# Performance work log

Measured on AMD Instinct MI355X. Metric: run time of the kernel, lower is better.

The kernel has to match this reference:

```python
import jax, jax.numpy as jnp
import numpy as np

B, T, S, D, H, HD, DFF, NB = 2, 2048, 2048, 768, 12, 64, 3072, 32
HID = H * HD
EPS = 1e-6
NEG = -1e9


def rmsnorm(x, w):
    # T5 RMSNorm: no mean subtraction, no bias
    var = jnp.mean(jnp.square(x), axis=-1, keepdims=True)
    return x * jax.lax.rsqrt(var + EPS) * w


def sdpa(h, kv, m, wq, wk, wv, wo):
    # h: [B,Tq,D], kv: [B,Tk,D], m: additive mask broadcastable to [B,H,Tq,Tk]
    b, tq, _ = h.shape
    tk = kv.shape[1]
    q = (h @ wq).reshape(b, tq, H, HD)
    k = (kv @ wk).reshape(b, tk, H, HD)
    v = (kv @ wv).reshape(b, tk, H, HD)
    scores = jnp.einsum('bthd,bshd->bhts', q, k) + m  # scale=1.0 (T5)
    p = jax.nn.softmax(scores, axis=-1)
    y = jnp.einsum('bhts,bshd->bthd', p, v).reshape(b, tq, HID)
    return y @ wo


def setup_inputs() -> dict:
    key = jax.random.key(0)
    ks = jax.random.split(key, 16)
    x = jax.random.normal(ks[0], (B, T, D), dtype=jnp.float32)
    # causal additive mask for decoder self-attention
    causal = jnp.tril(jnp.ones((T, T), dtype=bool))
    mask = jnp.broadcast_to(jnp.where(causal, 0.0, NEG)[None, None], (B, 1, T, T)).astype(jnp.float32)
    relative_position = jax.random.randint(ks[1], (1, 1, T, T), 0, NB)
    encoder_hidden_states = jax.random.normal(ks[2], (B, S, D), dtype=jnp.float32)
    encoder_attention_mask = jnp.zeros((B, 1, T, S), dtype=jnp.float32)
    sc = 0.02
    p = {
        'sn_w': jnp.ones((D,), jnp.float32),
        'wq': sc * jax.random.normal(ks[3], (D, HID)),
        'wk': sc * jax.random.normal(ks[4], (D, HID)),
        'wv': sc * jax.random.normal(ks[5], (D, HID)),
        'wo': sc * jax.random.normal(ks[6], (HID, D)),
        'rel_emb': sc * jax.random.normal(ks[7], (NB, H)),
        'cn_w': jnp.ones((D,), jnp.float32),
        'cwq': sc * jax.random.normal(ks[8], (D, HID)),
        'cwk': sc * jax.random.normal(ks[9], (D, HID)),
        'cwv': sc * jax.random.normal(ks[10], (D, HID)),
        'cwo': sc * jax.random.normal(ks[11], (HID, D)),
        'pn_w': jnp.ones((D,), jnp.float32),
        'ffn_wi': sc * jax.random.normal(ks[12], (D, DFF)),
        'ffn_wo': sc * jax.random.normal(ks[13], (DFF, D)),
    }
    return dict(x=x, mask=mask, relative_position=relative_position,
                encoder_hidden_states=encoder_hidden_states,
                encoder_attention_mask=encoder_attention_mask, **p)


def reference(x, mask, relative_position, encoder_hidden_states, encoder_attention_mask,
              sn_w, wq, wk, wv, wo, rel_emb, cn_w, cwq, cwk, cwv, cwo, pn_w, ffn_wi, ffn_wo):
    # self-attention with relative-position bias added into additive mask
    h = rmsnorm(x, sn_w)
    # rel_emb[relative_position]: [1,1,T,T,H] -> permute(0,1,4,2,3) -> squeeze(0) -> [1,H,T,T]
    position_bias = jnp.transpose(rel_emb[relative_position], (0, 1, 4, 2, 3))[0]
    self_mask = mask + position_bias
    y = sdpa(h, h, self_mask, wq, wk, wv, wo)
    attn_out = y + x
    # cross-attention (no relative bias -> zeros position bias)
    enc_dec_position_bias = jnp.zeros_like(encoder_attention_mask)
    h2 = rmsnorm(attn_out, cn_w)
    y2 = sdpa(h2, encoder_hidden_states, encoder_attention_mask + enc_dec_position_bias,
              cwq, cwk, cwv, cwo)
    attn_out = y2 + attn_out
    # T5 FFN: relu(x @ wi) @ wo, pre-norm, residual
    hn = rmsnorm(attn_out, pn_w)
    ff = jax.nn.relu(hn @ ffn_wi) @ ffn_wo
    return (attn_out + ff, position_bias, enc_dec_position_bias)
```

## Files before the change

kernel.cpp:

```cpp
#include <hip/hip_runtime.h>
#include <hip/hip_bf16.h>
#include <stdint.h>

#define T5_B   2
#define T5_T   2048
#define T5_S   2048
#define T5_D   768
#define T5_H   12
#define T5_HD  64
#define T5_DFF 3072
#define T5_NB  32
#define NROW   4096

typedef __attribute__((ext_vector_type(8))) short bf16x8;
typedef __attribute__((ext_vector_type(4))) short short4v;
typedef __attribute__((ext_vector_type(4))) float f32x4;

__device__ __forceinline__ unsigned short f2bf(float x) {
  unsigned int u = __float_as_uint(x);
  unsigned int r = (u + 0x7FFFu + ((u >> 16) & 1u)) >> 16;
  return (unsigned short)r;
}

__device__ __forceinline__ void load_lds16(const void* g, void* l) {
  __builtin_amdgcn_global_load_lds(
      (__attribute__((address_space(1))) void*)(const_cast<void*>(g)),
      (__attribute__((address_space(3))) void*)(l), 16, 0, 0);
}

__device__ __forceinline__ unsigned cvt_pk_bf16(float lo_, float hi_) {
  unsigned d;
  asm("v_cvt_pk_bf16_f32 %0, %1, %2" : "=v"(d) : "v"(lo_), "v"(hi_));
  return d;
}

__device__ __forceinline__ f32x4 mfma16(short4v a, short4v b, f32x4 c) {
#if __has_builtin(__builtin_amdgcn_mfma_f32_16x16x16bf16_1k)
  return __builtin_amdgcn_mfma_f32_16x16x16bf16_1k(a, b, c, 0, 0, 0);
#else
  asm volatile("v_mfma_f32_16x16x16_bf16 %0, %1, %2, %0" : "+v"(c) : "v"(a), "v"(b));
  return c;
#endif
}

__device__ __forceinline__ int xcd_swz(int f, int nwg) {
  int q8 = nwg >> 3, r8 = nwg & 7, xcd = f & 7, base = f >> 3;
  return (xcd < r8 ? xcd * (q8 + 1) : r8 * (q8 + 1) + (xcd - r8) * q8) + base;
}

template <int TM, int TN, int EPI, int NBUF>
__device__ __forceinline__ void gemm_body(
    int f, int gx, int nwg,
    const unsigned short* __restrict__ A, const unsigned short* __restrict__ Bt,
    void* __restrict__ C, const float* __restrict__ res, int N, int K,
    unsigned short* LDS) {
  constexpr int WR = (TM >= 128) ? 2 : 1;
  constexpr int WC = 4 / WR;
  constexpr int AM = TM / WR / 16;
  constexpr int AN = TN / WC / 16;
  constexpr int CHA = TM / 8, CHB = TN / 8, CPW = (CHA + CHB) / 4;
  constexpr int BUFSH = (TM + TN) * 64;
  constexpr int DEPTH = NBUF - 1;
  const int tid = threadIdx.x, lane = tid & 63, wv = tid >> 6;
  const int lo = lane & 15, hi = lane >> 4;
  const int wr = wv / WC, wc = wv % WC;
  const int wg = xcd_swz(f, nwg);
  const int m0 = (wg / gx) * TM, n0 = (wg % gx) * TN;

  f32x4 acc[AM][AN];
#pragma unroll
  for (int i = 0; i < AM; ++i)
#pragma unroll
    for (int j = 0; j < AN; ++j) acc[i][j] = f32x4{0.f, 0.f, 0.f, 0.f};

  const int srr  = lane >> 3;
  const int scol = ((lane & 7) ^ srr) * 8;

  auto stage = [&](int k0, int bsel) {
    unsigned short* Ab = LDS + bsel * BUFSH;
    unsigned short* Bb = Ab + TM * 64;
#pragma unroll
    for (int j = 0; j < CPW; ++j) {
      int c = wv * CPW + j;
      if (c < CHA)
        load_lds16(A + (size_t)(m0 + c * 8 + srr) * K + k0 + scol, Ab + c * 512);
      else {
        int c2 = c - CHA;
        load_lds16(Bt + (size_t)(n0 + c2 * 8 + srr) * K + k0 + scol, Bb + c2 * 512);
      }
    }
  };

  const int nIt = K >> 6;
#pragma unroll
  for (int p = 0; p < DEPTH; ++p)
    if (p < nIt) stage(p << 6, p % NBUF);

  for (int it = 0; it < nIt; ++it) {
    const int bsel = it % NBUF;
    if (it + DEPTH < nIt) {
      stage((it + DEPTH) << 6, (it + DEPTH) % NBUF);
      asm volatile("s_waitcnt vmcnt(%0)" :: "n"(DEPTH * CPW) : "memory");
    } else if (it + 1 < nIt) {
      asm volatile("s_waitcnt vmcnt(%0)" :: "n"(CPW) : "memory");
    } else {
      asm volatile("s_waitcnt vmcnt(0)" ::: "memory");
    }
    __builtin_amdgcn_s_barrier();
    __builtin_amdgcn_sched_barrier(0);
    const unsigned short* Ab = LDS + bsel * BUFSH;
    const unsigned short* Bb = Ab + TM * 64;
#pragma unroll
    for (int kk = 0; kk < 2; ++kk) {
      bf16x8 af[AM], bfr[AN];
#pragma unroll
      for (int i = 0; i < AM; ++i) {
        int row = wr * (AM * 16) + i * 16 + lo;
        unsigned by = (unsigned)(row * 128) + ((unsigned)(((kk * 4 + hi) ^ (row & 7))) << 4);
        af[i] = *(const bf16x8*)((const char*)Ab + by);
      }
#pragma unroll
      for (int j = 0; j < AN; ++j) {
        int row = wc * (AN * 16) + j * 16 + lo;
        unsigned by = (unsigned)(row * 128) + ((unsigned)(((kk * 4 + hi) ^ (row & 7))) << 4);
        bfr[j] = *(const bf16x8*)((const char*)Bb + by);
      }
      __builtin_amdgcn_s_setprio(1);
#pragma unroll
      for (int i = 0; i < AM; ++i)
#pragma unroll
        for (int j = 0; j < AN; ++j)
          acc[i][j] = __builtin_amdgcn_mfma_f32_16x16x32_bf16(af[i], bfr[j], acc[i][j], 0, 0, 0);
      __builtin_amdgcn_s_setprio(0);
    }
    __builtin_amdgcn_sched_barrier(0);
    __builtin_amdgcn_s_barrier();
  }

#pragma unroll
  for (int mi = 0; mi < AM; ++mi)
#pragma unroll
    for (int ni = 0; ni < AN; ++ni) {
      int row = m0 + wr * (AM * 16) + mi * 16 + hi * 4;
      int col = n0 + wc * (AN * 16) + ni * 16 + lo;
#pragma unroll
      for (int r = 0; r < 4; ++r) {
        float v = acc[mi][ni][r];
        size_t idx = (size_t)(row + r) * N + col;
        if (EPI == 0) {
          ((unsigned short*)C)[idx] = f2bf(v);
        } else if (EPI == 1) {
          ((float*)C)[idx] = v + res[idx];
        } else {
          ((unsigned short*)C)[idx] = f2bf(fmaxf(v, 0.0f));
        }
      }
    }
}

template <int TM, int TN, int EPI, int NBUF>
__global__ __launch_bounds__(256)
void gemm_bt(const unsigned short* __restrict__ A, const unsigned short* __restrict__ Bt,
             void* __restrict__ C, const float* __restrict__ res, int N, int K) {
  __shared__ __align__(16) unsigned short LDS[NBUF * (TM + TN) * 64];
  int f = blockIdx.y * gridDim.x + blockIdx.x;
  gemm_body<TM, TN, EPI, NBUF>(f, gridDim.x, gridDim.x * gridDim.y, A, Bt, C, res, N, K, LDS);
}

struct PrepArgs {
  const float* wsrc[10];
  unsigned short* wdst[10];
  const float* enc; unsigned short* encb;
  const int* rp; unsigned char* rp8;
  const float* x; const float* snw; unsigned short* normb;
};

__global__ __launch_bounds__(256)
void prep_kernel(PrepArgs a) {
  __shared__ __align__(16) float tile[32][33];
  const int bid = blockIdx.x, tid = threadIdx.x;
  if (bid < 9216) {
    int widx, rem, Kd, Nd;
    if (bid < 4608)      { widx = bid / 576; rem = bid % 576;  Kd = 768;  Nd = 768;  }
    else if (bid < 6912) { widx = 8;         rem = bid - 4608; Kd = 768;  Nd = 3072; }
    else                 { widx = 9;         rem = bid - 6912; Kd = 3072; Nd = 768;  }
    const float* W = a.wsrc[widx];
    unsigned short* Wt = a.wdst[widx];
    int nb = Nd / 32;
    int n0 = (rem % nb) * 32, k0 = (rem / nb) * 32;
    int tx = tid & 31, ty = tid >> 5;
#pragma unroll
    for (int i = 0; i < 32; i += 8)
      tile[ty + i][tx] = W[(size_t)(k0 + ty + i) * Nd + n0 + tx];
    __syncthreads();
#pragma unroll
    for (int i = 0; i < 32; i += 8)
      Wt[(size_t)(n0 + ty + i) * Kd + k0 + tx] = f2bf(tile[tx][ty + i]);
  } else if (bid < 12288) {
    int i = (bid - 9216) * 256 + tid;
    float4 v = ((const float4*)a.enc)[i];
    unsigned long long pk = (unsigned long long)f2bf(v.x)
                          | ((unsigned long long)f2bf(v.y) << 16)
                          | ((unsigned long long)f2bf(v.z) << 32)
                          | ((unsigned long long)f2bf(v.w) << 48);
    *(unsigned long long*)(a.encb + (size_t)i * 4) = pk;
  } else if (bid < 13312) {
    int idx = (bid - 12288) * 256 + tid;
    const int4* src = (const int4*)(a.rp + (size_t)idx * 16);
    int4 v0 = src[0], v1 = src[1], v2 = src[2], v3 = src[3];
    uint4 o;
    o.x = (v0.x & 31) | ((v0.y & 31) << 8) | ((v0.z & 31) << 16) | ((v0.w & 31) << 24);
    o.y = (v1.x & 31) | ((v1.y & 31) << 8) | ((v1.z & 31) << 16) | ((v1.w & 31) << 24);
    o.z = (v2.x & 31) | ((v2.y & 31) << 8) | ((v2.z & 31) << 16) | ((v2.w & 31) << 24);
    o.w = (v3.x & 31) | ((v3.y & 31) << 8) | ((v3.z & 31) << 16) | ((v3.w & 31) << 24);
    ((uint4*)a.rp8)[idx] = o;
  } else {
    int row = bid - 13312;
    const float* r = a.x + (size_t)row * 768;
    float x0 = r[tid], x1 = r[tid + 256], x2 = r[tid + 512];
    float s = x0 * x0 + x1 * x1 + x2 * x2;
#pragma unroll
    for (int off = 32; off > 0; off >>= 1) s += __shfl_xor(s, off);
    float* wsm = &tile[0][0];
    int lane = tid & 63, wvv = tid >> 6;
    if (lane == 0) wsm[wvv] = s;
    __syncthreads();
    float tot = wsm[0] + wsm[1] + wsm[2] + wsm[3];
    float rinv = rsqrtf(tot * (1.0f / 768.0f) + 1e-6f);
    unsigned short* o = a.normb + (size_t)row * 768;
    o[tid]       = f2bf(x0 * rinv * a.snw[tid]);
    o[tid + 256] = f2bf(x1 * rinv * a.snw[tid + 256]);
    o[tid + 512] = f2bf(x2 * rinv * a.snw[tid + 512]);
  }
}

__global__ __launch_bounds__(256)
void rmsnorm_kernel(const float* __restrict__ in, const float* __restrict__ w,
                    unsigned short* __restrict__ out) {
  int row = blockIdx.x, tid = threadIdx.x;
  const float* r = in + (size_t)row * 768;
  float x0 = r[tid], x1 = r[tid + 256], x2 = r[tid + 512];
  float s = x0 * x0 + x1 * x1 + x2 * x2;
#pragma unroll
  for (int off = 32; off > 0; off >>= 1) s += __shfl_xor(s, off);
  __shared__ float ws_[4];
  int lane = tid & 63, wv = tid >> 6;
  if (lane == 0) ws_[wv] = s;
  __syncthreads();
  float tot = ws_[0] + ws_[1] + ws_[2] + ws_[3];
  float rinv = rsqrtf(tot * (1.0f / 768.0f) + 1e-6f);
  unsigned short* o = out + (size_t)row * 768;
  o[tid]       = f2bf(x0 * rinv * w[tid]);
  o[tid + 256] = f2bf(x1 * rinv * w[tid + 256]);
  o[tid + 512] = f2bf(x2 * rinv * w[tid + 512]);
}

struct Stage1Args {
  const unsigned short *normb, *wqkvT, *encb, *wckvT;
  unsigned short *qkv, *ckv;
  const int* rp; const float* rel;
  float *out1, *out2;
};

__global__ __launch_bounds__(256)
void stage1_kernel(Stage1Args a) {
  __shared__ __align__(16) unsigned short LDS[32768];
  const int bid = blockIdx.x, tid = threadIdx.x;
  if (bid < 576) {
    gemm_body<128, 128, 0, 2>(bid, 18, 576, a.normb, a.wqkvT, a.qkv, nullptr, 2304, 768, LDS);
  } else if (bid < 960) {
    gemm_body<128, 128, 0, 2>(bid - 576, 12, 384, a.encb, a.wckvT, a.ckv, nullptr, 1536, 768, LDS);
  } else {
    const int p = bid - 960;
    float* rl = (float*)LDS;
    for (int i = tid; i < 384; i += 256) rl[i] = a.rel[i];
    __syncthreads();
    int t = p >> 1;
    int s = (p & 1) * 1024 + tid * 4;
    int4 nb = *(const int4*)(a.rp + (size_t)t * 2048 + s);
#pragma unroll
    for (int h = 0; h < 12; ++h) {
      float4 v = make_float4(rl[nb.x * 12 + h], rl[nb.y * 12 + h],
                             rl[nb.z * 12 + h], rl[nb.w * 12 + h]);
      *(float4*)(a.out1 + ((size_t)h * 2048 + t) * 2048 + s) = v;
    }
    size_t zbase = ((size_t)p * 256 + tid) * 8;
    float4 z = make_float4(0.f, 0.f, 0.f, 0.f);
    *(float4*)(a.out2 + zbase)     = z;
    *(float4*)(a.out2 + zbase + 4) = z;
  }
}

__global__ __launch_bounds__(256)
void transpose_both_kernel(const unsigned short* __restrict__ v1,
                           const unsigned short* __restrict__ v2,
                           unsigned short* __restrict__ vT1,
                           unsigned short* __restrict__ vT2) {
  __shared__ __align__(16) unsigned short tile[64][72];
  int which = blockIdx.z >> 1, b = blockIdx.z & 1;
  const unsigned short* vin = which ? v2 : v1;
  int stride = which ? 1536 : 2304;
  unsigned short* vT = which ? vT2 : vT1;
  int t0 = blockIdx.x * 64, h = blockIdx.y;
  int tid = threadIdx.x;
  {
    int tl = tid >> 2, d0 = (tid & 3) * 16;
    const unsigned short* src = vin + (size_t)(b * 2048 + t0 + tl) * stride + h * 64 + d0;
    *(bf16x8*)&tile[tl][d0]     = *(const bf16x8*)src;
    *(bf16x8*)&tile[tl][d0 + 8] = *(const bf16x8*)(src + 8);
  }
  __syncthreads();
  {
    int d = tid >> 2, t1 = (tid & 3) * 16;
    unsigned short tmp[16] __attribute__((aligned(16)));
#pragma unroll
    for (int j = 0; j < 16; ++j) tmp[j] = tile[t1 + j][d];
    unsigned short* dst = vT + ((size_t)((b * 12 + h) * 64 + d)) * 2048 + t0 + t1;
    *(bf16x8*)dst       = *(bf16x8*)&tmp[0];
    *(bf16x8*)(dst + 8) = *(bf16x8*)&tmp[8];
  }
}

template <bool SELF>
__device__ __forceinline__ void attn_qcomp(
    const bf16x8& qf0, const bf16x8& qf1, f32x4* Oc, float& m_, float& l_,
    const unsigned* nb4, const float* rel_l, int qrow, bool edge, int s0,
    const unsigned short* Kb, const unsigned short* Vb, int lo, int hi) {
  f32x4 S[4];
  __builtin_amdgcn_s_setprio(1);
#pragma unroll
  for (int ct = 0; ct < 4; ++ct) {
    int krow = ct * 16 + lo;
    unsigned by0 = ((unsigned)(krow * 128 + hi * 16))      ^ ((unsigned)(krow & 7) << 4);
    unsigned by1 = ((unsigned)(krow * 128 + 64 + hi * 16)) ^ ((unsigned)(krow & 7) << 4);
    bf16x8 kf0 = *(const bf16x8*)((const char*)Kb + by0);
    bf16x8 kf1 = *(const bf16x8*)((const char*)Kb + by1);
    f32x4 sa = f32x4{0.f, 0.f, 0.f, 0.f};
    sa = __builtin_amdgcn_mfma_f32_16x16x32_bf16(kf0, qf0, sa, 0, 0, 0);
    sa = __builtin_amdgcn_mfma_f32_16x16x32_bf16(kf1, qf1, sa, 0, 0, 0);
    S[ct] = sa;
  }
  __builtin_amdgcn_s_setprio(0);

  if constexpr (SELF) {
#pragma unroll
    for (int ct = 0; ct < 4; ++ct) {
#pragma unroll
      for (int r = 0; r < 4; ++r) {
        int s = s0 + ct * 16 + hi * 4 + r;
        float sc = S[ct][r] + rel_l[(nb4[ct] >> (8 * r)) & 31u];
        if (edge && s > qrow) sc = -1e30f;
        S[ct][r] = sc;
      }
    }
  }

  float tm = S[0][0];
#pragma unroll
  for (int ct = 0; ct < 4; ++ct)
#pragma unroll
    for (int r = 0; r < 4; ++r) tm = fmaxf(tm, S[ct][r]);
  tm = fmaxf(tm, __shfl_xor(tm, 16));
  tm = fmaxf(tm, __shfl_xor(tm, 32));
  float mn = fmaxf(m_, tm);
  float alpha = __expf(m_ - mn);
  float rs = 0.f;
#pragma unroll
  for (int ct = 0; ct < 4; ++ct)
#pragma unroll
    for (int r = 0; r < 4; ++r) { float e = __expf(S[ct][r] - mn); S[ct][r] = e; rs += e; }
  rs += __shfl_xor(rs, 16);
  rs += __shfl_xor(rs, 32);
  l_ = l_ * alpha + rs;
  if (tm > m_) {
#pragma unroll
    for (int dt = 0; dt < 4; ++dt)
#pragma unroll
      for (int r = 0; r < 4; ++r) Oc[dt][r] *= alpha;
  }
  m_ = mn;

  short4v pf[4];
#pragma unroll
  for (int ct = 0; ct < 4; ++ct) {
    union { unsigned u[2]; short4v s; } cv;
    cv.u[0] = cvt_pk_bf16(S[ct][0], S[ct][1]);
    cv.u[1] = cvt_pk_bf16(S[ct][2], S[ct][3]);
    pf[ct] = cv.s;
  }

  __builtin_amdgcn_s_setprio(1);
#pragma unroll
  for (int dt = 0; dt < 4; ++dt) {
    int vrow = dt * 16 + lo;
#pragma unroll
    for (int ct = 0; ct < 4; ++ct) {
      unsigned vb = ((unsigned)(vrow * 128 + ct * 32 + hi * 8)) ^ ((unsigned)(vrow & 7) << 4);
      short4v vf = *(const short4v*)((const char*)Vb + vb);
      Oc[dt] = mfma16(vf, pf[ct], Oc[dt]);
    }
  }
  __builtin_amdgcn_s_setprio(0);
}

__device__ __forceinline__ void attn_store(f32x4* Oc, float l_, unsigned short* yr) {
  float inv = 1.0f / l_;
#pragma unroll
  for (int dt = 0; dt < 4; ++dt) {
    unsigned long long pk = (unsigned long long)f2bf(Oc[dt][0] * inv)
                          | ((unsigned long long)f2bf(Oc[dt][1] * inv) << 16)
                          | ((unsigned long long)f2bf(Oc[dt][2] * inv) << 32)
                          | ((unsigned long long)f2bf(Oc[dt][3] * inv) << 48);
    *(unsigned long long*)(yr + dt * 16) = pk;
  }
}

__global__ __launch_bounds__(256)
void attn_self_kernel(const unsigned short* __restrict__ qp,
                      const unsigned short* __restrict__ kp,
                      const unsigned short* __restrict__ vT,
                      const unsigned char* __restrict__ rp8,
                      const float* __restrict__ rel_emb,
                      unsigned short* __restrict__ yp) {
  __shared__ __align__(16) unsigned short Kls[2][4096];
  __shared__ __align__(16) unsigned short Vls[2][4096];
  __shared__ float rel_l[32];

  const int tid = threadIdx.x, lane = tid & 63, wv = tid >> 6;
  const int lo = lane & 15, hi = lane >> 4;
  const int wg = xcd_swz(blockIdx.x + 32 * (blockIdx.y + 12 * blockIdx.z), 768);
  const int qt = 31 - (wg & 31);
  const int h = (wg >> 5) % 12, b = (wg >> 5) / 12;
  const int ntiles = qt + 1;

  if (tid < 32) rel_l[tid] = rel_emb[tid * 12 + h];

  const int q = qt * 64 + wv * 16 + lo;
  const unsigned short* qr = qp + (size_t)(b * T5_T + q) * 2304 + h * 64 + hi * 8;
  const bf16x8 qf0 = *(const bf16x8*)qr;
  const bf16x8 qf1 = *(const bf16x8*)(qr + 32);
  const unsigned char* rpq = rp8 + (size_t)q * 2048 + hi * 4;

  f32x4 Oc[4];
  float m_ = -3.0e38f, l_ = 0.f;
#pragma unroll
  for (int i = 0; i < 4; ++i) Oc[i] = f32x4{0.f, 0.f, 0.f, 0.f};

  const int krr = lane >> 3;
  const int kd0 = ((lane & 7) ^ krr) * 8;

  auto stage = [&](int kt, int bsel) {
    const int s0 = kt * 64;
#pragma unroll
    for (int j = 0; j < 2; ++j) {
      int c = wv * 2 + j;
      int rr = c * 8 + krr;
      load_lds16(kp + (size_t)(b * 2048 + s0 + rr) * 2304 + h * 64 + kd0, &Kls[bsel][c * 512]);
      load_lds16(vT + (size_t)((b * 12 + h) * 64 + rr) * 2048 + s0 + kd0,  &Vls[bsel][c * 512]);
    }
  };

  stage(0, 0);

  for (int kt = 0; kt < ntiles; ++kt) {
    const int bsel = kt & 1;
    const int s0 = kt * 64;
    asm volatile("s_waitcnt vmcnt(0)" ::: "memory");
    __syncthreads();
    unsigned nb4[4];
#pragma unroll
    for (int ct = 0; ct < 4; ++ct)
      nb4[ct] = *(const unsigned*)(rpq + s0 + ct * 16);
    if (kt + 1 < ntiles) stage(kt + 1, bsel ^ 1);

    attn_qcomp<true>(qf0, qf1, Oc, m_, l_, nb4, rel_l, q, kt == qt, s0,
                     &Kls[bsel][0], &Vls[bsel][0], lo, hi);
  }

#if !__has_builtin(__builtin_amdgcn_mfma_f32_16x16x16bf16_1k)
  asm volatile("s_nop 7\n\ts_nop 7" ::: );
#endif

  attn_store(Oc, l_, yp + (size_t)(b * T5_T + q) * 768 + h * 64 + hi * 4);
}

__global__ __launch_bounds__(256)
void attn_cross_kernel(const unsigned short* __restrict__ qp,
                       const unsigned short* __restrict__ kp,
                       const unsigned short* __restrict__ vT,
                       unsigned short* __restrict__ yp) {
  __shared__ __align__(16) unsigned short Kls[2][4096];
  __shared__ __align__(16) unsigned short Vls[2][4096];

  const int tid = threadIdx.x, lane = tid & 63, wv = tid >> 6;
  const int lo = lane & 15, hi = lane >> 4;
  const int wg = xcd_swz(blockIdx.x + 32 * (blockIdx.y + 12 * blockIdx.z), 768);
  const int xq = wg & 31, h = (wg >> 5) % 12, b = (wg >> 5) / 12;

  const int q = xq * 64 + wv * 16 + lo;
  const unsigned short* qr = qp + (size_t)(b * T5_T + q) * 768 + h * 64 + hi * 8;
  const bf16x8 qf0 = *(const bf16x8*)qr;
  const bf16x8 qf1 = *(const bf16x8*)(qr + 32);

  f32x4 Oc[4];
  float m_ = -3.0e38f, l_ = 0.f;
#pragma unroll
  for (int i = 0; i < 4; ++i) Oc[i] = f32x4{0.f, 0.f, 0.f, 0.f};

  const int krr = lane >> 3;
  const int kd0 = ((lane & 7) ^ krr) * 8;

  auto stage = [&](int kt, int bsel) {
    const int s0 = kt * 64;
#pragma unroll
    for (int j = 0; j < 2; ++j) {
      int c = wv * 2 + j;
      int rr = c * 8 + krr;
      load_lds16(kp + (size_t)(b * 2048 + s0 + rr) * 1536 + h * 64 + kd0, &Kls[bsel][c * 512]);
      load_lds16(vT + (size_t)((b * 12 + h) * 64 + rr) * 2048 + s0 + kd0, &Vls[bsel][c * 512]);
    }
  };

  stage(0, 0);

  for (int kt = 0; kt < 32; ++kt) {
    const int bsel = kt & 1;
    asm volatile("s_waitcnt vmcnt(0)" ::: "memory");
    __syncthreads();
    if (kt + 1 < 32) stage(kt + 1, bsel ^ 1);
    attn_qcomp<false>(qf0, qf1, Oc, m_, l_, nullptr, nullptr, 0, false, kt * 64,
                      &Kls[bsel][0], &Vls[bsel][0], lo, hi);
  }

#if !__has_builtin(__builtin_amdgcn_mfma_f32_16x16x16bf16_1k)
  asm volatile("s_nop 7\n\ts_nop 7" ::: );
#endif

  attn_store(Oc, l_, yp + (size_t)(b * T5_T + q) * 768 + h * 64 + hi * 4);
}

extern "C" void kernel_launch(void* const* d_in, const int* in_sizes, int n_in,
                              void* d_out, int out_size, void* d_ws, size_t ws_size,
                              hipStream_t stream) {
  (void)in_sizes; (void)n_in; (void)out_size; (void)ws_size;
  const float* x    = (const float*)d_in[0];
  const int*   rp   = (const int*)d_in[2];
  const float* enc  = (const float*)d_in[3];
  const float* sn_w = (const float*)d_in[5];
  const float* wq   = (const float*)d_in[6];
  const float* wk   = (const float*)d_in[7];
  const float* wvw  = (const float*)d_in[8];
  const float* wo   = (const float*)d_in[9];
  const float* rel  = (const float*)d_in[10];
  const float* cn_w = (const float*)d_in[11];
  const float* cwq  = (const float*)d_in[12];
  const float* cwk  = (const float*)d_in[13];
  const float* cwv  = (const float*)d_in[14];
  const float* cwo  = (const float*)d_in[15];
  const float* pn_w = (const float*)d_in[16];
  const float* wi   = (const float*)d_in[17];
  const float* wo2  = (const float*)d_in[18];

  float* out0 = (float*)d_out;
  float* out1 = out0 + (size_t)NROW * T5_D;
  float* out2 = out1 + (size_t)T5_H * T5_T * T5_T;

  char* ws = (char*)d_ws;
  size_t off = 0;
  auto alloc = [&](size_t bytes) { char* p = ws + off; off += (bytes + 255) & ~(size_t)255; return p; };
  unsigned short* wqkvT = (unsigned short*)alloc((size_t)2304 * 768 * 2);
  unsigned short* woT   = (unsigned short*)alloc((size_t)768 * 768 * 2);
  unsigned short* wckvT = (unsigned short*)alloc((size_t)1536 * 768 * 2);
  unsigned short* wcqT  = (unsigned short*)alloc((size_t)768 * 768 * 2);
  unsigned short* wcoT  = (unsigned short*)alloc((size_t)768 * 768 * 2);
  unsigned short* wiT   = (unsigned short*)alloc((size_t)3072 * 768 * 2);
  unsigned short* woT2  = (unsigned short*)alloc((size_t)768 * 3072 * 2);
  unsigned short* normb = (unsigned short*)alloc((size_t)NROW * 768 * 2);
  unsigned short* encb  = (unsigned short*)alloc((size_t)NROW * 768 * 2);
  unsigned short* ybuf  = (unsigned short*)alloc((size_t)NROW * 768 * 2);
  unsigned short* cq    = (unsigned short*)alloc((size_t)NROW * 768 * 2);
  float*          attn  = (float*)alloc((size_t)NROW * 768 * 4);
  unsigned char*  rp8p  = (unsigned char*)alloc((size_t)2048 * 2048);
  unsigned short* qkv   = (unsigned short*)alloc((size_t)NROW * 2304 * 2);
  unsigned short* ckv   = (unsigned short*)alloc((size_t)NROW * 1536 * 2);
  unsigned short* vT1   = (unsigned short*)alloc((size_t)24 * 64 * 2048 * 2);
  unsigned short* vT2   = (unsigned short*)alloc((size_t)24 * 64 * 2048 * 2);
  unsigned short* ffh   = (unsigned short*)alloc((size_t)NROW * 3072 * 2);

  dim3 blk(256);

  {
    PrepArgs pa;
    pa.wsrc[0] = wq;  pa.wdst[0] = wqkvT;
    pa.wsrc[1] = wk;  pa.wdst[1] = wqkvT + 768 * 768;
    pa.wsrc[2] = wvw; pa.wdst[2] = wqkvT + 2 * 768 * 768;
    pa.wsrc[3] = wo;  pa.wdst[3] = woT;
    pa.wsrc[4] = cwk; pa.wdst[4] = wckvT;
    pa.wsrc[5] = cwv; pa.wdst[5] = wckvT + 768 * 768;
    pa.wsrc[6] = cwq; pa.wdst[6] = wcqT;
    pa.wsrc[7] = cwo; pa.wdst[7] = wcoT;
    pa.wsrc[8] = wi;  pa.wdst[8] = wiT;
    pa.wsrc[9] = wo2; pa.wdst[9] = woT2;
    pa.enc = enc; pa.encb = encb; pa.rp = rp; pa.rp8 = rp8p;
    pa.x = x; pa.snw = sn_w; pa.normb = normb;
    prep_kernel<<<17408, blk, 0, stream>>>(pa);
  }

  {
    Stage1Args sa;
    sa.normb = normb; sa.wqkvT = wqkvT; sa.encb = encb; sa.wckvT = wckvT;
    sa.qkv = qkv; sa.ckv = ckv; sa.rp = rp; sa.rel = rel;
    sa.out1 = out1; sa.out2 = out2;
    stage1_kernel<<<5056, blk, 0, stream>>>(sa);
  }

  transpose_both_kernel<<<dim3(32, 12, 4), blk, 0, stream>>>(qkv + 1536, ckv + 768, vT1, vT2);

  attn_self_kernel<<<dim3(32, 12, 2), blk, 0, stream>>>(qkv, qkv + 768, vT1, rp8p, rel, ybuf);
  gemm_bt<64, 64, 1, 3><<<dim3(12, 64), blk, 0, stream>>>(ybuf, woT, attn, x, 768, 768);

  rmsnorm_kernel<<<NROW, blk, 0, stream>>>(attn, cn_w, normb);
  gemm_bt<64, 64, 0, 3><<<dim3(12, 64), blk, 0, stream>>>(normb, wcqT, cq, nullptr, 768, 768);
  attn_cross_kernel<<<dim3(32, 12, 2), blk, 0, stream>>>(cq, ckv, vT2, ybuf);
  gemm_bt<64, 64, 1, 3><<<dim3(12, 64), blk, 0, stream>>>(ybuf, wcoT, attn, attn, 768, 768);

  rmsnorm_kernel<<<NROW, blk, 0, stream>>>(attn, pn_w, normb);
  gemm_bt<128, 128, 2, 2><<<dim3(24, 32), blk, 0, stream>>>(normb, wiT, ffh, nullptr, 3072, 768);
  gemm_bt<64, 64, 1, 3><<<dim3(12, 64), blk, 0, stream>>>(ffh, woT2, out0, attn, 768, 3072);
}
```

Baseline: 366.1 us.

## Fuse V transpose into projection GEMM epilogue and pair causal query tiles

The QKV and cross-KV projection GEMMs now write the V columns directly in transposed per-head layout, so the separate transpose kernel and its extra read and write of V are gone. The causal self-attention kernel now has each workgroup process two query tiles (tile i and tile 31-i) over one shared K/V stream. This balances the causal work across workgroups, halves the grid and reuses the staged K/V tiles for both query tiles. The transposed epilogue does strided 8-byte stores, and carrying two accumulator sets raises register pressure.

```diff
diff --git a/kernel.cpp b/kernel.cpp
--- a/kernel.cpp
+++ b/kernel.cpp
@@ -53,7 +53,7 @@
     int f, int gx, int nwg,
     const unsigned short* __restrict__ A, const unsigned short* __restrict__ Bt,
     void* __restrict__ C, const float* __restrict__ res, int N, int K,
-    unsigned short* LDS) {
+    unsigned short* LDS, unsigned short* vtp = nullptr, int vcol0 = 0) {
   constexpr int WR = (TM >= 128) ? 2 : 1;
   constexpr int WC = 4 / WR;
   constexpr int AM = TM / WR / 16;
@@ -143,16 +143,26 @@
     for (int ni = 0; ni < AN; ++ni) {
       int row = m0 + wr * (AM * 16) + mi * 16 + hi * 4;
       int col = n0 + wc * (AN * 16) + ni * 16 + lo;
-#pragma unroll
-      for (int r = 0; r < 4; ++r) {
-        float v = acc[mi][ni][r];
-        size_t idx = (size_t)(row + r) * N + col;
-        if (EPI == 0) {
-          ((unsigned short*)C)[idx] = f2bf(v);
-        } else if (EPI == 1) {
-          ((float*)C)[idx] = v + res[idx];
-        } else {
-          ((unsigned short*)C)[idx] = f2bf(fmaxf(v, 0.0f));
+      if (EPI == 3 && col >= vcol0) {
+        int cc = col - vcol0, hh = cc >> 6, dd = cc & 63;
+        int bb = row >> 11, tt = row & 2047;
+        unsigned long long pk = (unsigned long long)f2bf(acc[mi][ni][0])
+                              | ((unsigned long long)f2bf(acc[mi][ni][1]) << 16)
+                              | ((unsigned long long)f2bf(acc[mi][ni][2]) << 32)
+                              | ((unsigned long long)f2bf(acc[mi][ni][3]) << 48);
+        *(unsigned long long*)(vtp + ((size_t)((bb * 12 + hh) * 64 + dd)) * 2048 + tt) = pk;
+      } else {
+#pragma unroll
+        for (int r = 0; r < 4; ++r) {
+          float v = acc[mi][ni][r];
+          size_t idx = (size_t)(row + r) * N + col;
+          if (EPI == 0 || EPI == 3) {
+            ((unsigned short*)C)[idx] = f2bf(v);
+          } else if (EPI == 1) {
+            ((float*)C)[idx] = v + res[idx];
+          } else {
+            ((unsigned short*)C)[idx] = f2bf(fmaxf(v, 0.0f));
+          }
         }
       }
     }
@@ -257,7 +267,7 @@
 
 struct Stage1Args {
   const unsigned short *normb, *wqkvT, *encb, *wckvT;
-  unsigned short *qkv, *ckv;
+  unsigned short *qkv, *ckv, *vT1, *vT2;
   const int* rp; const float* rel;
   float *out1, *out2;
 };
@@ -267,9 +277,11 @@
   __shared__ __align__(16) unsigned short LDS[32768];
   const int bid = blockIdx.x, tid = threadIdx.x;
   if (bid < 576) {
-    gemm_body<128, 128, 0, 2>(bid, 18, 576, a.normb, a.wqkvT, a.qkv, nullptr, 2304, 768, LDS);
+    gemm_body<128, 128, 3, 2>(bid, 18, 576, a.normb, a.wqkvT, a.qkv, nullptr, 2304, 768,
+                              LDS, a.vT1, 1536);
   } else if (bid < 960) {
-    gemm_body<128, 128, 0, 2>(bid - 576, 12, 384, a.encb, a.wckvT, a.ckv, nullptr, 1536, 768, LDS);
+    gemm_body<128, 128, 3, 2>(bid - 576, 12, 384, a.encb, a.wckvT, a.ckv, nullptr, 1536, 768,
+                              LDS, a.vT2, 768);
   } else {
     const int p = bid - 960;
     float* rl = (float*)LDS;
@@ -288,36 +300,6 @@
     float4 z = make_float4(0.f, 0.f, 0.f, 0.f);
     *(float4*)(a.out2 + zbase)     = z;
     *(float4*)(a.out2 + zbase + 4) = z;
-  }
-}
-
-__global__ __launch_bounds__(256)
-void transpose_both_kernel(const unsigned short* __restrict__ v1,
-                           const unsigned short* __restrict__ v2,
-                           unsigned short* __restrict__ vT1,
-                           unsigned short* __restrict__ vT2) {
-  __shared__ __align__(16) unsigned short tile[64][72];
-  int which = blockIdx.z >> 1, b = blockIdx.z & 1;
-  const unsigned short* vin = which ? v2 : v1;
-  int stride = which ? 1536 : 2304;
-  unsigned short* vT = which ? vT2 : vT1;
-  int t0 = blockIdx.x * 64, h = blockIdx.y;
-  int tid = threadIdx.x;
-  {
-    int tl = tid >> 2, d0 = (tid & 3) * 16;
-    const unsigned short* src = vin + (size_t)(b * 2048 + t0 + tl) * stride + h * 64 + d0;
-    *(bf16x8*)&tile[tl][d0]     = *(const bf16x8*)src;
-    *(bf16x8*)&tile[tl][d0 + 8] = *(const bf16x8*)(src + 8);
-  }
-  __syncthreads();
-  {
-    int d = tid >> 2, t1 = (tid & 3) * 16;
-    unsigned short tmp[16] __attribute__((aligned(16)));
-#pragma unroll
-    for (int j = 0; j < 16; ++j) tmp[j] = tile[t1 + j][d];
-    unsigned short* dst = vT + ((size_t)((b * 12 + h) * 64 + d)) * 2048 + t0 + t1;
-    *(bf16x8*)dst       = *(bf16x8*)&tmp[0];
-    *(bf16x8*)(dst + 8) = *(bf16x8*)&tmp[8];
   }
 }
 
@@ -428,23 +410,28 @@
 
   const int tid = threadIdx.x, lane = tid & 63, wv = tid >> 6;
   const int lo = lane & 15, hi = lane >> 4;
-  const int wg = xcd_swz(blockIdx.x + 32 * (blockIdx.y + 12 * blockIdx.z), 768);
-  const int qt = 31 - (wg & 31);
-  const int h = (wg >> 5) % 12, b = (wg >> 5) / 12;
-  const int ntiles = qt + 1;
+  const int wg = xcd_swz(blockIdx.x + 16 * (blockIdx.y + 12 * blockIdx.z), 384);
+  const int xq = wg & 15, h = (wg >> 4) % 12, b = (wg >> 4) / 12;
+  const int qta = xq, qtb = 31 - xq;
+  const int ntiles = qtb + 1;
 
   if (tid < 32) rel_l[tid] = rel_emb[tid * 12 + h];
 
-  const int q = qt * 64 + wv * 16 + lo;
-  const unsigned short* qr = qp + (size_t)(b * T5_T + q) * 2304 + h * 64 + hi * 8;
-  const bf16x8 qf0 = *(const bf16x8*)qr;
-  const bf16x8 qf1 = *(const bf16x8*)(qr + 32);
-  const unsigned char* rpq = rp8 + (size_t)q * 2048 + hi * 4;
-
-  f32x4 Oc[4];
-  float m_ = -3.0e38f, l_ = 0.f;
-#pragma unroll
-  for (int i = 0; i < 4; ++i) Oc[i] = f32x4{0.f, 0.f, 0.f, 0.f};
+  const int qA = qta * 64 + wv * 16 + lo;
+  const int qB = qtb * 64 + wv * 16 + lo;
+  const unsigned short* qrA = qp + (size_t)(b * T5_T + qA) * 2304 + h * 64 + hi * 8;
+  const unsigned short* qrB = qp + (size_t)(b * T5_T + qB) * 2304 + h * 64 + hi * 8;
+  const bf16x8 qa0 = *(const bf16x8*)qrA;
+  const bf16x8 qa1 = *(const bf16x8*)(qrA + 32);
+  const bf16x8 qb0 = *(const bf16x8*)qrB;
+  const bf16x8 qb1 = *(const bf16x8*)(qrB + 32);
+  const unsigned char* rpqA = rp8 + (size_t)qA * 2048 + hi * 4;
+  const unsigned char* rpqB = rp8 + (size_t)qB * 2048 + hi * 4;
+
+  f32x4 OA[4], OB[4];
+  float mA = -3.0e38f, lA = 0.f, mB = -3.0e38f, lB = 0.f;
+#pragma unroll
+  for (int i = 0; i < 4; ++i) { OA[i] = f32x4{0.f, 0.f, 0.f, 0.f}; OB[i] = f32x4{0.f, 0.f, 0.f, 0.f}; }
 
   const int krr = lane >> 3;
   const int kd0 = ((lane & 7) ^ krr) * 8;
@@ -467,21 +454,29 @@
     const int s0 = kt * 64;
     asm volatile("s_waitcnt vmcnt(0)" ::: "memory");
     __syncthreads();
-    unsigned nb4[4];
-#pragma unroll
-    for (int ct = 0; ct < 4; ++ct)
-      nb4[ct] = *(const unsigned*)(rpq + s0 + ct * 16);
+    unsigned nbA[4], nbB[4];
+    if (kt <= qta) {
+#pragma unroll
+      for (int ct = 0; ct < 4; ++ct) nbA[ct] = *(const unsigned*)(rpqA + s0 + ct * 16);
+    }
+#pragma unroll
+    for (int ct = 0; ct < 4; ++ct) nbB[ct] = *(const unsigned*)(rpqB + s0 + ct * 16);
     if (kt + 1 < ntiles) stage(kt + 1, bsel ^ 1);
 
-    attn_qcomp<true>(qf0, qf1, Oc, m_, l_, nb4, rel_l, q, kt == qt, s0,
-                     &Kls[bsel][0], &Vls[bsel][0], lo, hi);
+    const unsigned short* Kb = &Kls[bsel][0];
+    const unsigned short* Vb = &Vls[bsel][0];
+
+    if (kt <= qta)
+      attn_qcomp<true>(qa0, qa1, OA, mA, lA, nbA, rel_l, qA, kt == qta, s0, Kb, Vb, lo, hi);
+    attn_qcomp<true>(qb0, qb1, OB, mB, lB, nbB, rel_l, qB, kt == qtb, s0, Kb, Vb, lo, hi);
   }
 
 #if !__has_builtin(__builtin_amdgcn_mfma_f32_16x16x16bf16_1k)
   asm volatile("s_nop 7\n\ts_nop 7" ::: );
 #endif
 
-  attn_store(Oc, l_, yp + (size_t)(b * T5_T + q) * 768 + h * 64 + hi * 4);
+  attn_store(OA, lA, yp + (size_t)(b * T5_T + qA) * 768 + h * 64 + hi * 4);
+  attn_store(OB, lB, yp + (size_t)(b * T5_T + qB) * 768 + h * 64 + hi * 4);
 }
 
 __global__ __launch_bounds__(256)
@@ -609,14 +604,12 @@
   {
     Stage1Args sa;
     sa.normb = normb; sa.wqkvT = wqkvT; sa.encb = encb; sa.wckvT = wckvT;
-    sa.qkv = qkv; sa.ckv = ckv; sa.rp = rp; sa.rel = rel;
-    sa.out1 = out1; sa.out2 = out2;
+    sa.qkv = qkv; sa.ckv = ckv; sa.vT1 = vT1; sa.vT2 = vT2;
+    sa.rp = rp; sa.rel = rel; sa.out1 = out1; sa.out2 = out2;
     stage1_kernel<<<5056, blk, 0, stream>>>(sa);
   }
 
-  transpose_both_kernel<<<dim3(32, 12, 4), blk, 0, stream>>>(qkv + 1536, ckv + 768, vT1, vT2);
-
-  attn_self_kernel<<<dim3(32, 12, 2), blk, 0, stream>>>(qkv, qkv + 768, vT1, rp8p, rel, ybuf);
+  attn_self_kernel<<<dim3(16, 12, 2), blk, 0, stream>>>(qkv, qkv + 768, vT1, rp8p, rel, ybuf);
   gemm_bt<64, 64, 1, 3><<<dim3(12, 64), blk, 0, stream>>>(ybuf, woT, attn, x, 768, 768);
 
   rmsnorm_kernel<<<NROW, blk, 0, stream>>>(attn, cn_w, normb);
```

Measured after the change: 352.2 us. 3.8% less time.
